# Optimization experiments

Measured on AMD Instinct MI355X. Metric: run time of the kernel, lower is better.

The kernel has to match this reference:

```python
import jax, jax.numpy as jnp
import numpy as np

GROUPS = 32
EPS = 1e-5
NHEAD = 8


def group_norm(x, gamma, beta):
    # x: [B, C, T]
    B, C, T = x.shape
    xg = x.reshape(B, GROUPS, C // GROUPS, T)
    mean = xg.mean(axis=(2, 3), keepdims=True)
    var = xg.var(axis=(2, 3), keepdims=True)
    xg = (xg - mean) * jax.lax.rsqrt(var + EPS)
    x = xg.reshape(B, C, T)
    return x * gamma[None, :, None] + beta[None, :, None]


def conv1x1(x, w, b):
    # x: [B, C_in, T], w: [C_out, C_in], b: [C_out]
    return jnp.einsum('oc,bct->bot', w, x) + b[None, :, None]


def setup_inputs() -> dict:
    key = jax.random.key(0)
    ks = jax.random.split(key, 4)
    B, C, T = 8, 512, 2048
    x = jax.random.normal(ks[0], (B, C, T), dtype=jnp.float32)
    w_qkv = jax.random.normal(ks[1], (3 * C, C), dtype=jnp.float32) * (1.0 / np.sqrt(C))
    b_qkv = jnp.zeros((3 * C,), dtype=jnp.float32)
    w_proj = jax.random.normal(ks[2], (C, C), dtype=jnp.float32) * (1.0 / np.sqrt(C))
    b_proj = jnp.zeros((C,), dtype=jnp.float32)
    return {
        'x': x,
        'gn1_gamma': jnp.ones((C,), jnp.float32), 'gn1_beta': jnp.zeros((C,), jnp.float32),
        'w_qkv': w_qkv, 'b_qkv': b_qkv,
        'gn2_gamma': jnp.ones((C,), jnp.float32), 'gn2_beta': jnp.zeros((C,), jnp.float32),
        'w_proj': w_proj, 'b_proj': b_proj,
    }


def qkv_attention(qkv):
    # qkv: [B, 3*H*ch, T] laid out as H blocks of (q ch, k ch, v ch)
    B, width, T = qkv.shape
    ch = width // (3 * NHEAD)
    qkv = qkv.reshape(B, NHEAD, 3 * ch, T)
    q, k, v = qkv[:, :, :ch], qkv[:, :, ch:2 * ch], qkv[:, :, 2 * ch:]
    scale = 1.0 / np.sqrt(np.sqrt(ch)).astype(np.float32)
    # scores: [B, H, T(q), T(k)]
    w = jnp.einsum('bhct,bhcs->bhts', q * scale, k * scale)
    w = jax.nn.softmax(w, axis=-1)  # max-subtract softmax, same math
    a = jnp.einsum('bhts,bhcs->bhct', w, v)
    return a.reshape(B, NHEAD * ch, T)


def reference(x, gn1_gamma, gn1_beta, w_qkv, b_qkv, gn2_gamma, gn2_beta, w_proj, b_proj):
    # x: [B, C, T]
    qkv = conv1x1(group_norm(x, gn1_gamma, gn1_beta), w_qkv, b_qkv)  # [B, 3C, T]
    h = qkv_attention(qkv)                                            # [B, C, T]
    h = conv1x1(group_norm(h, gn2_gamma, gn2_beta), w_proj, b_proj)   # [B, C, T]
    return x + h
```

## Files before the change

### kernel.cpp

```cpp
#include <hip/hip_runtime.h>

typedef unsigned short u16;
typedef unsigned int   u32;
typedef __attribute__((ext_vector_type(8))) short short8;
typedef __attribute__((ext_vector_type(4))) float floatx4;

__device__ inline u16 f2bf(float x) {
  union { float f; unsigned u; } v; v.f = x;
  unsigned r = v.u + 0x7FFFu + ((v.u >> 16) & 1u);
  return (u16)(r >> 16);
}
__device__ inline float bf2f(short s) {
  union { u32 u; float f; } v; v.u = ((u32)(u16)s) << 16; return v.f;
}
__device__ inline short8 ld8(const u16* p) {
  return *reinterpret_cast<const short8*>(p);
}
__device__ inline void async_ld16(const u16* g, u16* l) {
  unsigned loff = (unsigned)(unsigned long long)(void*)l;
  __builtin_amdgcn_global_load_lds(reinterpret_cast<const unsigned*>(g),
      reinterpret_cast<__attribute__((address_space(3))) unsigned*>(loff), 16, 0, 0);
}

__global__ __launch_bounds__(1024) void gncast(const float* __restrict__ x,
                                               const float* __restrict__ gamma,
                                               const float* __restrict__ beta,
                                               u16* __restrict__ xn,
                                               const float* __restrict__ wq,
                                               u16* __restrict__ wqb,
                                               const float* __restrict__ wp,
                                               u16* __restrict__ wpb) {
  __shared__ u16 tile[16 * 2048];
  float* stats = (float*)tile;
  const int tid = threadIdx.x;
  if (blockIdx.x >= 256) {
    int i = (blockIdx.x - 256) * 1024 + tid;
    const float* src; u16* dst; int j;
    if (i < 196608) { src = wq; dst = wqb; j = i; }
    else            { src = wp; dst = wpb; j = i - 196608; }
    float4 v = reinterpret_cast<const float4*>(src)[j];
    union { u16 u[4]; float2 f; } w;
    w.u[0] = f2bf(v.x); w.u[1] = f2bf(v.y); w.u[2] = f2bf(v.z); w.u[3] = f2bf(v.w);
    reinterpret_cast<float2*>(dst)[j] = w.f;
    return;
  }
  int b = blockIdx.x >> 5, g = blockIdx.x & 31;
  const float* base = x + ((long)b * 512 + g * 16) * 2048;
  float s = 0.f, ss = 0.f;
  for (int i = tid; i < 8192; i += 1024) {
    float4 v = reinterpret_cast<const float4*>(base)[i];
    s  += v.x + v.y + v.z + v.w;
    ss += v.x * v.x + v.y * v.y + v.z * v.z + v.w * v.w;
    int c = i >> 9, t4 = (i & 511) * 4;
    union { u16 u[4]; float2 f; } w;
    w.u[0] = f2bf(v.x); w.u[1] = f2bf(v.y); w.u[2] = f2bf(v.z); w.u[3] = f2bf(v.w);
    *reinterpret_cast<float2*>(&tile[c * 2048 + t4]) = w.f;
  }
  #pragma unroll
  for (int d = 1; d < 64; d <<= 1) { s += __shfl_xor(s, d); ss += __shfl_xor(ss, d); }
  __syncthreads();
  int wave = tid >> 6, lane = tid & 63;
  if (lane == 0) { stats[wave] = s; stats[wave + 16] = ss; }
  __syncthreads();
  s = 0.f; ss = 0.f;
  #pragma unroll
  for (int w = 0; w < 16; w++) { s += stats[w]; ss += stats[w + 16]; }
  float mean = s * (1.f / 32768.f);
  float var  = ss * (1.f / 32768.f) - mean * mean;
  float rstd = rsqrtf(var + 1e-5f);
  float ga[16], be[16];
  #pragma unroll
  for (int c = 0; c < 16; c++) {
    float gm = gamma[g * 16 + c];
    ga[c] = gm * rstd;
    be[c] = beta[g * 16 + c] - mean * rstd * gm;
  }
  u16* ob = xn + (long)b * 2048 * 512 + g * 16;
  #pragma unroll
  for (int tt = 0; tt < 2; tt++) {
    int t = tid * 2 + tt;
    union { u16 u[8]; float4 f; } w0, w1;
    #pragma unroll
    for (int c = 0; c < 16; c++) {
      float f;
      if (c == 0 && t < 64) f = base[t];
      else                  f = bf2f((short)tile[c * 2048 + t]);
      u16 o = f2bf(f * ga[c] + be[c]);
      if (c < 8) w0.u[c] = o; else w1.u[c - 8] = o;
    }
    u16* dst = ob + (long)t * 512;
    *reinterpret_cast<float4*>(dst)     = w0.f;
    *reinterpret_cast<float4*>(dst + 8) = w1.f;
  }
}

__global__ __launch_bounds__(1024) void gn_tc(const u16* __restrict__ a,
                                              const float* __restrict__ gamma,
                                              const float* __restrict__ beta,
                                              u16* __restrict__ hn) {
  int b = blockIdx.x >> 5, g = blockIdx.x & 31;
  const u16* base = a + (long)b * 2048 * 512 + g * 16;
  float s = 0.f, ss = 0.f;
  for (int t = threadIdx.x; t < 2048; t += 1024) {
    const u16* p = base + (long)t * 512;
    short8 v0 = ld8(p), v1 = ld8(p + 8);
    #pragma unroll
    for (int j = 0; j < 8; j++) {
      float f0 = bf2f(v0[j]), f1 = bf2f(v1[j]);
      s += f0 + f1; ss += f0 * f0 + f1 * f1;
    }
  }
  #pragma unroll
  for (int d = 1; d < 64; d <<= 1) { s += __shfl_xor(s, d); ss += __shfl_xor(ss, d); }
  __shared__ float red[32];
  int wave = threadIdx.x >> 6, lane = threadIdx.x & 63;
  if (lane == 0) { red[wave] = s; red[wave + 16] = ss; }
  __syncthreads();
  s = 0.f; ss = 0.f;
  #pragma unroll
  for (int w = 0; w < 16; w++) { s += red[w]; ss += red[w + 16]; }
  float mean = s * (1.f / 32768.f);
  float var  = ss * (1.f / 32768.f) - mean * mean;
  float rstd = rsqrtf(var + 1e-5f);
  float ga[16], be[16];
  #pragma unroll
  for (int c = 0; c < 16; c++) {
    float gm = gamma[g * 16 + c];
    ga[c] = gm * rstd;
    be[c] = beta[g * 16 + c] - mean * rstd * gm;
  }
  u16* ob = hn + (long)b * 2048 * 512 + g * 16;
  for (int t = threadIdx.x; t < 2048; t += 1024) {
    const u16* p = base + (long)t * 512;
    short8 v0 = ld8(p), v1 = ld8(p + 8);
    union { u16 u[8]; float4 f; } w0, w1;
    #pragma unroll
    for (int c = 0; c < 8; c++)  w0.u[c] = f2bf(bf2f(v0[c]) * ga[c] + be[c]);
    #pragma unroll
    for (int c = 0; c < 8; c++)  w1.u[c] = f2bf(bf2f(v1[c]) * ga[c + 8] + be[c + 8]);
    u16* dst = ob + (long)t * 512;
    *reinterpret_cast<float4*>(dst)     = w0.f;
    *reinterpret_cast<float4*>(dst + 8) = w1.f;
  }
}

template<int QKV>
__global__ __launch_bounds__(256) void gemm_tn(
    const u16* __restrict__ A, long abst,
    const u16* __restrict__ Bt, long bbst,
    const float* __restrict__ bias,
    const float* __restrict__ resid, long rbst,
    void* __restrict__ outp, long obst,
    u16* __restrict__ vtp, int K) {
  __shared__ __align__(16) u16 As[2][128 * 32];
  __shared__ __align__(16) u16 Bs[2][128 * 32];
  const int tid = threadIdx.x;
  const int m0 = blockIdx.y * 128, n0 = blockIdx.x * 128;
  const int N = gridDim.x * 128;
  const long bz = blockIdx.z;
  const u16* Ab = A + bz * abst + (long)m0 * K;
  const u16* Bb = Bt + bz * bbst + (long)n0 * K;
  const int lane = tid & 63, wave = tid >> 6;
  const int wm = (wave & 1) * 64, wn = (wave >> 1) * 64;
  const int l15 = lane & 15, quad = lane >> 4;
  const u16* ag[2]; const u16* bg[2];
  const int ldso = wave * 512;
  #pragma unroll
  for (int half = 0; half < 2; half++) {
    int r = half * 64 + (tid >> 2);
    ag[half] = Ab + (long)r * K + (tid & 3) * 8;
    bg[half] = Bb + (long)r * K + (tid & 3) * 8;
  }

  floatx4 acc[4][4];
  #pragma unroll
  for (int i = 0; i < 4; i++)
    #pragma unroll
    for (int j = 0; j < 4; j++) acc[i][j] = (floatx4){0.f, 0.f, 0.f, 0.f};

  #pragma unroll
  for (int half = 0; half < 2; half++) {
    async_ld16(ag[half], &As[0][half * 2048 + ldso]);
    async_ld16(bg[half], &Bs[0][half * 2048 + ldso]);
  }
  const int nk = K >> 5;
  for (int ki = 0; ki < nk; ki++) {
    __syncthreads();
    if (ki + 1 < nk) {
      int k1 = (ki + 1) << 5, bsel = (ki + 1) & 1;
      #pragma unroll
      for (int half = 0; half < 2; half++) {
        async_ld16(ag[half] + k1, &As[bsel][half * 2048 + ldso]);
        async_ld16(bg[half] + k1, &Bs[bsel][half * 2048 + ldso]);
      }
    }
    const u16* as = As[ki & 1]; const u16* bs = Bs[ki & 1];
    short8 af[4], bfr[4];
    #pragma unroll
    for (int i = 0; i < 4; i++) af[i]  = ld8(&as[(wm + i * 16 + l15) * 32 + quad * 8]);
    #pragma unroll
    for (int i = 0; i < 4; i++) bfr[i] = ld8(&bs[(wn + i * 16 + l15) * 32 + quad * 8]);
    #pragma unroll
    for (int mi = 0; mi < 4; mi++)
      #pragma unroll
      for (int ni = 0; ni < 4; ni++)
        acc[mi][ni] = __builtin_amdgcn_mfma_f32_16x16x32_bf16(af[mi], bfr[ni], acc[mi][ni], 0, 0, 0);
  }

  if (QKV) {
    u16* D  = (u16*)outp + bz * obst;
    u16* VT = vtp + bz * (8L * 64 * 2048);
    #pragma unroll
    for (int ni = 0; ni < 4; ni++) {
      int nb = n0 + wn + ni * 16;
      int region = (nb >> 6) % 3;
      int n = nb + l15;
      float bn = bias[n];
      if (region == 2) {
        int hh = n / 192, c = (n % 192) - 128;
        u16* vrow = VT + ((long)hh * 64 + c) * 2048 + m0 + wm;
        #pragma unroll
        for (int mi = 0; mi < 4; mi++) {
          union { u16 u[4]; float2 f; } pk;
          #pragma unroll
          for (int r = 0; r < 4; r++) pk.u[r] = f2bf(acc[mi][ni][r] + bn);
          *reinterpret_cast<float2*>(vrow + mi * 16 + quad * 4) = pk.f;
        }
      } else {
        float sc = (region == 0) ? 0.180336880f : 1.f;
        #pragma unroll
        for (int mi = 0; mi < 4; mi++)
          #pragma unroll
          for (int r = 0; r < 4; r++) {
            int m = m0 + wm + mi * 16 + quad * 4 + r;
            D[(long)m * 1536 + n] = f2bf((acc[mi][ni][r] + bn) * sc);
          }
      }
    }
  } else {
    float* D = (float*)outp + bz * obst;
    const float* R = resid + bz * rbst;
    #pragma unroll
    for (int mi = 0; mi < 4; mi++)
      #pragma unroll
      for (int r = 0; r < 4; r++) {
        int m = m0 + wm + mi * 16 + quad * 4 + r;
        float bm = bias[m];
        #pragma unroll
        for (int ni = 0; ni < 4; ni++) {
          int n = n0 + wn + ni * 16 + l15;
          long idx = (long)m * N + n;
          D[idx] = acc[mi][ni][r] + bm + R[idx];
        }
      }
  }
}

__global__ __launch_bounds__(256, 2) void attn(const u16* __restrict__ qkv,
                                               const u16* __restrict__ vt,
                                               u16* __restrict__ aout) {
  __shared__ __align__(16) u16 Ps[256 * 64];
  __shared__ __align__(16) u16 Ks[2][64 * 64];
  __shared__ __align__(16) u16 Vs[2][64 * 64];
  const int tid = threadIdx.x, lane = tid & 63, wave = tid >> 6;
  const int l15 = lane & 15, quad = lane >> 4;
  const int sw = l15 & 7;
  const int bh = blockIdx.x & 63;
  const int b = bh >> 3, h = bh & 7;
  const int t0 = (blockIdx.x >> 6) * 256;
  const u16* qbase = qkv + (long)b * 2048 * 1536 + h * 192;
  const u16* vbase = vt + (long)(b * 8 + h) * 64 * 2048;

  short8 qf[4][2];
  #pragma unroll
  for (int tqi = 0; tqi < 4; tqi++)
    #pragma unroll
    for (int ks = 0; ks < 2; ks++)
      qf[tqi][ks] = ld8(qbase + (long)(t0 + wave * 64 + tqi * 16 + l15) * 1536 + ks * 32 + quad * 8);

  short8 ones;
  #pragma unroll
  for (int j = 0; j < 8; j++) ones[j] = (short)0x3F80;

  const u16* kg[2]; const u16* vg[2]; int ldso[2];
  #pragma unroll
  for (int half = 0; half < 2; half++) {
    int p = half * 256 + wave * 64 + lane;
    int row = p >> 3, c = (p & 7) ^ (row & 7);
    kg[half] = qbase + (long)row * 1536 + 64 + c * 8;
    vg[half] = vbase + (long)row * 2048 + c * 8;
    ldso[half] = (half * 256 + wave * 64) * 8;
  }
  #pragma unroll
  for (int half = 0; half < 2; half++) {
    async_ld16(kg[half], &Ks[0][ldso[half]]);
    async_ld16(vg[half], &Vs[0][ldso[half]]);
  }

  floatx4 accO[4][4];
  floatx4 lacc[4];
  #pragma unroll
  for (int ci = 0; ci < 4; ci++)
    #pragma unroll
    for (int tqi = 0; tqi < 4; tqi++) accO[ci][tqi] = (floatx4){0.f, 0.f, 0.f, 0.f};
  #pragma unroll
  for (int tqi = 0; tqi < 4; tqi++) lacc[tqi] = (floatx4){0.f, 0.f, 0.f, 0.f};

  for (int it = 0; it < 32; it++) {
    const u16* kb = Ks[it & 1];
    const u16* vb = Vs[it & 1];
    __syncthreads();
    if (it < 31) {
      int s1 = (it + 1) * 64;
      u16* kn = Ks[(it & 1) ^ 1];
      u16* vn = Vs[(it & 1) ^ 1];
      #pragma unroll
      for (int half = 0; half < 2; half++) {
        async_ld16(kg[half] + (long)s1 * 1536, &kn[ldso[half]]);
        async_ld16(vg[half] + s1,              &vn[ldso[half]]);
      }
    }

    floatx4 sacc[4][4];
    #pragma unroll
    for (int i = 0; i < 4; i++)
      #pragma unroll
      for (int j = 0; j < 4; j++) sacc[i][j] = (floatx4){0.f, 0.f, 0.f, 0.f};
    #pragma unroll
    for (int ks = 0; ks < 2; ks++) {
      short8 kf[4];
      #pragma unroll
      for (int tki = 0; tki < 4; tki++)
        kf[tki] = ld8(&kb[((tki * 16 + l15) << 6) + (((ks * 4 + quad) ^ sw) << 3)]);
      #pragma unroll
      for (int tki = 0; tki < 4; tki++)
        #pragma unroll
        for (int tqi = 0; tqi < 4; tqi++)
          sacc[tki][tqi] = __builtin_amdgcn_mfma_f32_16x16x32_bf16(kf[tki], qf[tqi][ks], sacc[tki][tqi], 0, 0, 0);
    }

    #pragma unroll
    for (int tqi = 0; tqi < 4; tqi++) {
      int prow = (wave * 64 + tqi * 16 + l15) << 6;
      #pragma unroll
      for (int tki = 0; tki < 4; tki++) {
        float p0 = __builtin_amdgcn_exp2f(sacc[tki][tqi][0]);
        float p1 = __builtin_amdgcn_exp2f(sacc[tki][tqi][1]);
        float p2 = __builtin_amdgcn_exp2f(sacc[tki][tqi][2]);
        float p3 = __builtin_amdgcn_exp2f(sacc[tki][tqi][3]);
        union { u32 u[2]; float2 f; } pk;
        pk.u[0] = __builtin_amdgcn_perm(__float_as_uint(p1), __float_as_uint(p0), 0x07060302);
        pk.u[1] = __builtin_amdgcn_perm(__float_as_uint(p3), __float_as_uint(p2), 0x07060302);
        int c16 = tki * 2 + (quad >> 1);
        *reinterpret_cast<float2*>(
            &Ps[prow + ((c16 ^ sw) << 3) + ((quad & 1) << 2)]) = pk.f;
      }
    }

    #pragma unroll
    for (int ks = 0; ks < 2; ks++) {
      short8 vf[4], pf[4];
      #pragma unroll
      for (int ci = 0; ci < 4; ci++)
        vf[ci] = ld8(&vb[((ci * 16 + l15) << 6) + (((ks * 4 + quad) ^ sw) << 3)]);
      #pragma unroll
      for (int tqi = 0; tqi < 4; tqi++)
        pf[tqi] = ld8(&Ps[((wave * 64 + tqi * 16 + l15) << 6) + (((ks * 4 + quad) ^ sw) << 3)]);
      #pragma unroll
      for (int tqi = 0; tqi < 4; tqi++)
        lacc[tqi] = __builtin_amdgcn_mfma_f32_16x16x32_bf16(ones, pf[tqi], lacc[tqi], 0, 0, 0);
      #pragma unroll
      for (int ci = 0; ci < 4; ci++)
        #pragma unroll
        for (int tqi = 0; tqi < 4; tqi++)
          accO[ci][tqi] = __builtin_amdgcn_mfma_f32_16x16x32_bf16(vf[ci], pf[tqi], accO[ci][tqi], 0, 0, 0);
    }
  }

  u16* ob = aout + ((long)b * 2048 + t0 + wave * 64) * 512 + h * 64;
  #pragma unroll
  for (int tqi = 0; tqi < 4; tqi++) {
    float invl = 1.f / lacc[tqi][0];
    #pragma unroll
    for (int ci = 0; ci < 4; ci++) {
      union { u16 u[4]; float2 f; } pk;
      #pragma unroll
      for (int r = 0; r < 4; r++) pk.u[r] = f2bf(accO[ci][tqi][r] * invl);
      *reinterpret_cast<float2*>(ob + (long)(tqi * 16 + l15) * 512 + ci * 16 + quad * 4) = pk.f;
    }
  }
}

extern "C" void kernel_launch(void* const* d_in, const int* in_sizes, int n_in,
                              void* d_out, int out_size, void* d_ws, size_t ws_size,
                              hipStream_t stream) {
  const float* x   = (const float*)d_in[0];
  const float* g1  = (const float*)d_in[1];
  const float* be1 = (const float*)d_in[2];
  const float* wq  = (const float*)d_in[3];
  const float* bq  = (const float*)d_in[4];
  const float* g2  = (const float*)d_in[5];
  const float* be2 = (const float*)d_in[6];
  const float* wp  = (const float*)d_in[7];
  const float* bp  = (const float*)d_in[8];

  char* ws = (char*)d_ws;
  u16*   xn   = (u16*)ws;
  u16*   a    = (u16*)ws;
  u16*   qkvb = (u16*)(ws + 33554432);
  u16*   hn   = (u16*)(ws + 83886080);
  u16*   vtb  = hn;
  u16*   wqb  = (u16*)(ws + 100663296);
  u16*   wpb  = (u16*)(ws + 102236160);

  gncast<<<512, 1024, 0, stream>>>(x, g1, be1, xn, wq, wqb, wp, wpb);
  gemm_tn<1><<<dim3(12, 16, 8), 256, 0, stream>>>(
      xn, (long)2048 * 512, wqb, 0, bq, nullptr, 0, qkvb, (long)2048 * 1536, vtb, 512);
  attn<<<512, 256, 0, stream>>>(qkvb, vtb, a);
  gn_tc<<<256, 1024, 0, stream>>>(a, g2, be2, hn);
  gemm_tn<0><<<dim3(16, 4, 8), 256, 0, stream>>>(
      wpb, 0, hn, (long)2048 * 512, bp, x, (long)512 * 2048, d_out, (long)512 * 2048, nullptr, 512);
}
```

Before: 267.7 us.

## Keep attention probabilities in registers via permlane swaps instead of LDS

Removes the 32KB shared-memory staging buffer for the softmax probabilities P. The exp2 results are packed to bf16 and rearranged across lanes with permlane32/permlane16 swaps into the B-operand layout of the PV MFMA. This cuts LDS writes and reads per key tile and lowers LDS footprint, which could raise occupancy. In exchange it adds cross-lane permute instructions, and the lane mapping has to match the earlier layout exactly.

```diff
diff --git a/kernel.cpp b/kernel.cpp
--- a/kernel.cpp
+++ b/kernel.cpp
@@ -259,7 +259,6 @@
 __global__ __launch_bounds__(256, 2) void attn(const u16* __restrict__ qkv,
                                                const u16* __restrict__ vt,
                                                u16* __restrict__ aout) {
-  __shared__ __align__(16) u16 Ps[256 * 64];
   __shared__ __align__(16) u16 Ks[2][64 * 64];
   __shared__ __align__(16) u16 Vs[2][64 * 64];
   const int tid = threadIdx.x, lane = tid & 63, wave = tid >> 6;
@@ -340,22 +339,12 @@
     }
 
     #pragma unroll
-    for (int tqi = 0; tqi < 4; tqi++) {
-      int prow = (wave * 64 + tqi * 16 + l15) << 6;
-      #pragma unroll
-      for (int tki = 0; tki < 4; tki++) {
-        float p0 = __builtin_amdgcn_exp2f(sacc[tki][tqi][0]);
-        float p1 = __builtin_amdgcn_exp2f(sacc[tki][tqi][1]);
-        float p2 = __builtin_amdgcn_exp2f(sacc[tki][tqi][2]);
-        float p3 = __builtin_amdgcn_exp2f(sacc[tki][tqi][3]);
-        union { u32 u[2]; float2 f; } pk;
-        pk.u[0] = __builtin_amdgcn_perm(__float_as_uint(p1), __float_as_uint(p0), 0x07060302);
-        pk.u[1] = __builtin_amdgcn_perm(__float_as_uint(p3), __float_as_uint(p2), 0x07060302);
-        int c16 = tki * 2 + (quad >> 1);
-        *reinterpret_cast<float2*>(
-            &Ps[prow + ((c16 ^ sw) << 3) + ((quad & 1) << 2)]) = pk.f;
-      }
-    }
+    for (int tki = 0; tki < 4; tki++)
+      #pragma unroll
+      for (int tqi = 0; tqi < 4; tqi++)
+        #pragma unroll
+        for (int r = 0; r < 4; r++)
+          sacc[tki][tqi][r] = __builtin_amdgcn_exp2f(sacc[tki][tqi][r]);
 
     #pragma unroll
     for (int ks = 0; ks < 2; ks++) {
@@ -364,8 +353,23 @@
       for (int ci = 0; ci < 4; ci++)
         vf[ci] = ld8(&vb[((ci * 16 + l15) << 6) + (((ks * 4 + quad) ^ sw) << 3)]);
       #pragma unroll
-      for (int tqi = 0; tqi < 4; tqi++)
-        pf[tqi] = ld8(&Ps[((wave * 64 + tqi * 16 + l15) << 6) + (((ks * 4 + quad) ^ sw) << 3)]);
+      for (int tqi = 0; tqi < 4; tqi++) {
+        u32 a0 = __builtin_amdgcn_perm(__float_as_uint(sacc[2 * ks][tqi][1]),
+                                       __float_as_uint(sacc[2 * ks][tqi][0]), 0x07060302);
+        u32 a1 = __builtin_amdgcn_perm(__float_as_uint(sacc[2 * ks][tqi][3]),
+                                       __float_as_uint(sacc[2 * ks][tqi][2]), 0x07060302);
+        u32 b0 = __builtin_amdgcn_perm(__float_as_uint(sacc[2 * ks + 1][tqi][1]),
+                                       __float_as_uint(sacc[2 * ks + 1][tqi][0]), 0x07060302);
+        u32 b1 = __builtin_amdgcn_perm(__float_as_uint(sacc[2 * ks + 1][tqi][3]),
+                                       __float_as_uint(sacc[2 * ks + 1][tqi][2]), 0x07060302);
+        auto u0 = __builtin_amdgcn_permlane32_swap(a0, b0, false, false);
+        auto v0 = __builtin_amdgcn_permlane16_swap(u0[0], u0[1], false, false);
+        auto u1 = __builtin_amdgcn_permlane32_swap(a1, b1, false, false);
+        auto v1 = __builtin_amdgcn_permlane16_swap(u1[0], u1[1], false, false);
+        union { u32 w[4]; short8 s8; } pw;
+        pw.w[0] = v0[0]; pw.w[1] = v1[0]; pw.w[2] = v0[1]; pw.w[3] = v1[1];
+        pf[tqi] = pw.s8;
+      }
       #pragma unroll
       for (int tqi = 0; tqi < 4; tqi++)
         lacc[tqi] = __builtin_amdgcn_mfma_f32_16x16x32_bf16(ones, pf[tqi], lacc[tqi], 0, 0, 0);
```

Result: no change. 265.8 us (-0.7%).
